# Kernel optimization log

Measured on AMD Instinct MI355X. Metric: run time of the kernel, lower is better.

## Reference

```python
import jax, jax.numpy as jnp
import numpy as np

N = 50000      # nodes
E = 800000     # edges
F = 128        # num_features
H = 128        # hidden_channels
L = 3          # num_layers
P = 32         # num_partitions
EPS = 1e-5     # BatchNorm1d eps


def _batchnorm(h):
    # BatchNorm1d(affine=False, track_running_stats=False): batch stats, biased var
    m = jnp.mean(h, axis=0)
    v = jnp.var(h, axis=0)
    return (h - m) * jax.lax.rsqrt(v + EPS)


def setup_inputs() -> dict:
    key = jax.random.key(0)
    ks = jax.random.split(key, 12)
    x = jax.random.normal(ks[0], (N, F), dtype=jnp.float32)
    edge_index = jax.random.randint(ks[1], (2, E), 0, N)
    edge_weights = jax.random.uniform(ks[2], (E,), dtype=jnp.float32)
    partitions = (jax.random.uniform(ks[3], (N, P)) < (1.0 / P)).astype(jnp.float32)
    node_weights = jax.random.uniform(ks[4], (N,), dtype=jnp.float32)
    edge_curr_node = jax.random.uniform(ks[5], (N,), dtype=jnp.float32)
    conv_w = 0.05 * jax.random.normal(ks[6], (L, F, H), dtype=jnp.float32)
    conv_b = jnp.zeros((L, H), dtype=jnp.float32)
    lin1_w = 0.05 * jax.random.normal(ks[7], (4 * H, H), dtype=jnp.float32)
    lin1_b = jnp.zeros((H,), dtype=jnp.float32)
    lin2_w = 0.05 * jax.random.normal(ks[8], (H, 1), dtype=jnp.float32)
    lin2_b = jnp.zeros((1,), dtype=jnp.float32)
    return {"x": x, "edge_index": edge_index, "edge_weights": edge_weights,
            "partitions": partitions, "node_weights": node_weights,
            "edge_curr_node": edge_curr_node, "conv_w": conv_w, "conv_b": conv_b,
            "lin1_w": lin1_w, "lin1_b": lin1_b, "lin2_w": lin2_w,
            "lin2_b": lin2_b, "curr_node_id": 123}


def reference(x, edge_index, edge_weights, partitions, node_weights,
              edge_curr_node, conv_w, conv_b, lin1_w, lin1_b, lin2_w, lin2_b,
              curr_node_id):
    src, dst = edge_index[0], edge_index[1]
    # GCN normalization with added self-loops (weight 1)
    deg = jax.ops.segment_sum(edge_weights, dst, num_segments=N) + 1.0
    dinv = jax.lax.rsqrt(deg)
    norm = dinv[src] * edge_weights * dinv[dst]          # [E]
    self_norm = (dinv * dinv)[:, None]                   # [N,1]

    h = x
    for l in range(L):
        hw = h @ conv_w[l] + conv_b[l]                   # [N,H]
        agg = jax.ops.segment_sum(hw[src] * norm[:, None], dst, num_segments=N)
        agg = agg + hw * self_norm                       # self-loop term
        h = jax.nn.relu(_batchnorm(agg))

    x_curr = h[curr_node_id]                             # [H]
    # mlp scoring: concat [h | x_curr | edge_col repeated to 2H] -> [N,4H]
    cat = jnp.concatenate([
        h,
        jnp.broadcast_to(x_curr[None, :], (N, H)),
        jnp.broadcast_to(edge_curr_node[:, None], (N, 2 * H)),
    ], axis=1)
    scores = jax.nn.relu(cat @ lin1_w + lin1_b) @ lin2_w + lin2_b  # [N,1]
    # pool == 'sum'
    partition_scores = scores.T @ partitions             # [1,P]
    return (partition_scores, h)
```

## Files before the change

### kernel.cpp

```cpp
#include <hip/hip_runtime.h>

#define N_NODES 50000
#define N_EDGES 800000
#define NP 50048
#define MAXDEG 64
#define PADK 136
#define NCOPY 64
#define EB 3125
#define WPB 512

typedef __bf16 bf16_8 __attribute__((ext_vector_type(8)));
typedef float  f32_4  __attribute__((ext_vector_type(4)));

__device__ inline float2 bf2f2(unsigned int u) {
    union { unsigned int i; float f; } a, b;
    a.i = u << 16;
    b.i = u & 0xffff0000u;
    return make_float2(a.f, b.f);
}

__global__ void k_init_wprep(int* __restrict__ fillp, float* __restrict__ colpart,
                             float* __restrict__ out_head,
                             const float* __restrict__ conv_w, const float* __restrict__ lin1_w,
                             __bf16* __restrict__ WT, float* __restrict__ svec) {
    int b = blockIdx.x;
    if (b < EB) {
        int i = b * 256 + threadIdx.x;
        fillp[i] = 0;
        if (i < 2 * NCOPY * 128) colpart[i] = 0.f;
        if (i < 32) out_head[i] = 0.f;
    } else if (b < EB + WPB) {
        int b2 = b - EB;
        int mat = b2 >> 7, n = b2 & 127, k = threadIdx.x;
        if (k < 128) {
            const float* srcm = (mat < 3) ? (conv_w + (size_t)mat * 16384) : lin1_w;
            WT[((size_t)mat * 128 + n) * 128 + k] = (__bf16)srcm[(size_t)k * 128 + n];
        }
    } else {
        int j = threadIdx.x;
        if (j < 128) {
            float s = 0.f;
            for (int k = 256; k < 512; ++k) s += lin1_w[(size_t)k * 128 + j];
            svec[j] = s;
        }
    }
}

__global__ void k_fillover(const int* __restrict__ src, const int* __restrict__ dst,
                           const float* __restrict__ ew,
                           int* __restrict__ fillp, uint2* __restrict__ esn) {
    int e = blockIdx.x * 256 + threadIdx.x;
    if (e >= N_EDGES) return;
    int d = dst[e];
    int pos = atomicAdd(&fillp[d * 16], 1);
    if (pos < MAXDEG)
        esn[(size_t)d * MAXDEG + pos] = make_uint2((unsigned)src[e], __float_as_uint(ew[e]));
}

__global__ void k_node(const uint2* __restrict__ esn, const int* __restrict__ fillp,
                       float* __restrict__ dinv) {
    int n = blockIdx.x * 256 + threadIdx.x;
    if (n >= N_NODES) return;
    int c = min(fillp[n * 16], MAXDEG);
    float s = 1.0f;
    for (int i = 0; i < c; ++i) s += __uint_as_float(esn[(size_t)n * MAXDEG + i].y);
    dinv[n] = rsqrtf(s);
}

template <int AMODE>
__global__ __launch_bounds__(256) void k_gemm_mfma(const float* __restrict__ A,
                                                   const float* __restrict__ mean,
                                                   const float* __restrict__ rstd,
                                                   const __bf16* __restrict__ WT,
                                                   const float* __restrict__ bias,
                                                   __bf16* __restrict__ C, int nrows) {
    __shared__ __bf16 As[64 * PADK];
    __shared__ __bf16 Ws[128 * PADK];
    int t = threadIdx.x;
    int rowBase = blockIdx.x * 64;
    const uint4* WTg = (const uint4*)WT;
    for (int i = t; i < 2048; i += 256) {
        int n = i >> 4, k8 = i & 15;
        *(uint4*)&Ws[n * PADK + k8 * 8] = WTg[i];
    }
    const float4* A4 = (const float4*)A;
    const float4* M4 = (const float4*)mean;
    const float4* R4 = (const float4*)rstd;
    for (int i = t; i < 1024; i += 256) {
        int r = i >> 4, k8 = i & 15;
        int gr = rowBase + r;
        float4 a0 = make_float4(0.f, 0.f, 0.f, 0.f), a1 = a0;
        if (gr < nrows) {
            a0 = A4[(size_t)gr * 32 + k8 * 2];
            a1 = A4[(size_t)gr * 32 + k8 * 2 + 1];
        }
        if (AMODE == 1) {
            float4 m0 = M4[k8 * 2], m1 = M4[k8 * 2 + 1];
            float4 r0 = R4[k8 * 2], r1 = R4[k8 * 2 + 1];
            a0.x = fmaxf((a0.x - m0.x) * r0.x, 0.f); a0.y = fmaxf((a0.y - m0.y) * r0.y, 0.f);
            a0.z = fmaxf((a0.z - m0.z) * r0.z, 0.f); a0.w = fmaxf((a0.w - m0.w) * r0.w, 0.f);
            a1.x = fmaxf((a1.x - m1.x) * r1.x, 0.f); a1.y = fmaxf((a1.y - m1.y) * r1.y, 0.f);
            a1.z = fmaxf((a1.z - m1.z) * r1.z, 0.f); a1.w = fmaxf((a1.w - m1.w) * r1.w, 0.f);
        }
        bf16_8 o = { (__bf16)a0.x, (__bf16)a0.y, (__bf16)a0.z, (__bf16)a0.w,
                     (__bf16)a1.x, (__bf16)a1.y, (__bf16)a1.z, (__bf16)a1.w };
        *(bf16_8*)&As[r * PADK + k8 * 8] = o;
    }
    __syncthreads();
    int wave = t >> 6, lane = t & 63, quad = lane >> 4, m = lane & 15;
    int ar = wave * 16 + m;
    f32_4 acc[8];
#pragma unroll
    for (int i = 0; i < 8; ++i) acc[i] = (f32_4){0.f, 0.f, 0.f, 0.f};
#pragma unroll
    for (int kk = 0; kk < 4; ++kk) {
        bf16_8 a = *(const bf16_8*)&As[ar * PADK + kk * 32 + quad * 8];
#pragma unroll
        for (int n0 = 0; n0 < 8; ++n0) {
            bf16_8 b = *(const bf16_8*)&Ws[(n0 * 16 + m) * PADK + kk * 32 + quad * 8];
            acc[n0] = __builtin_amdgcn_mfma_f32_16x16x32_bf16(a, b, acc[n0], 0, 0, 0);
        }
    }
    __syncthreads();
#pragma unroll
    for (int n0 = 0; n0 < 8; ++n0) {
        int col = n0 * 16 + m;
        float bi = bias[col];
#pragma unroll
        for (int r = 0; r < 4; ++r) {
            int rr = wave * 16 + quad * 4 + r;
            As[rr * PADK + col] = (__bf16)(acc[n0][r] + bi);
        }
    }
    __syncthreads();
    uint4* Cg = (uint4*)C;
    for (int i = t; i < 1024; i += 256) {
        int r = i >> 4, k8 = i & 15;
        int gr = rowBase + r;
        if (gr < nrows) Cg[(size_t)gr * 16 + k8] = *(const uint4*)&As[r * PADK + k8 * 8];
    }
}

__global__ __launch_bounds__(256) void k_agg(const __bf16* __restrict__ hwb,
                                             const uint2* __restrict__ esn,
                                             const int* __restrict__ fillp,
                                             const float* __restrict__ dinv,
                                             float* __restrict__ agg,
                                             float* __restrict__ colpart) {
    __shared__ float red1[4 * 128], red2[4 * 128];
    int t = threadIdx.x;
    int n = (blockIdx.x * 256 + t) >> 6;
    int lane = t & 63, wave = t >> 6;
    float2 acc = make_float2(0.f, 0.f);
    const unsigned int* hw32 = (const unsigned int*)hwb;
    if (n < N_NODES) {
        float dvn = dinv[n];
        float2 sv = bf2f2(hw32[(size_t)n * 64 + lane]);
        acc.x = sv.x * dvn * dvn; acc.y = sv.y * dvn * dvn;
        int num = min(fillp[n * 16], MAXDEG);
        int s_l = 0; float w_l = 0.f;
        if (lane < num) {
            uint2 e = esn[(size_t)n * MAXDEG + lane];
            s_l = (int)e.x;
            w_l = dinv[s_l] * __uint_as_float(e.y) * dvn;
        }
        int i = 0;
        for (; i + 8 <= num; i += 8) {
            int ss[8]; float ww[8]; unsigned uu[8];
#pragma unroll
            for (int j = 0; j < 8; ++j) { ss[j] = __shfl(s_l, i + j); ww[j] = __shfl(w_l, i + j); }
#pragma unroll
            for (int j = 0; j < 8; ++j) uu[j] = hw32[(size_t)ss[j] * 64 + lane];
#pragma unroll
            for (int j = 0; j < 8; ++j) {
                float2 f = bf2f2(uu[j]);
                acc.x += f.x * ww[j]; acc.y += f.y * ww[j];
            }
        }
        for (; i < num; ++i) {
            int s = __shfl(s_l, i);
            float w = __shfl(w_l, i);
            float2 f = bf2f2(hw32[(size_t)s * 64 + lane]);
            acc.x += f.x * w; acc.y += f.y * w;
        }
        ((float2*)agg)[(size_t)n * 64 + lane] = acc;
    }
    *(float2*)&red1[wave * 128 + 2 * lane] = acc;
    *(float2*)&red2[wave * 128 + 2 * lane] = make_float2(acc.x * acc.x, acc.y * acc.y);
    __syncthreads();
    if (t < 128) {
        float s = red1[t] + red1[128 + t] + red1[256 + t] + red1[384 + t];
        float q = red2[t] + red2[128 + t] + red2[256 + t] + red2[384 + t];
        int c = blockIdx.x & (NCOPY - 1);
        unsafeAtomicAdd(&colpart[c * 128 + t], s);
        unsafeAtomicAdd(&colpart[NCOPY * 128 + c * 128 + t], q);
    }
}

__global__ void k_bnfinal(float* colpart, float* mean, float* rstd) {
    int j = threadIdx.x;
    float s = 0.f, q = 0.f;
    for (int c = 0; c < NCOPY; ++c) {
        s += colpart[c * 128 + j];
        q += colpart[NCOPY * 128 + c * 128 + j];
        colpart[c * 128 + j] = 0.f;
        colpart[NCOPY * 128 + c * 128 + j] = 0.f;
    }
    float m = s * (1.0f / N_NODES);
    float v = q * (1.0f / N_NODES) - m * m;
    mean[j] = m;
    rstd[j] = rsqrtf(v + 1e-5f);
}

__global__ void k_prep(const float* __restrict__ agg, const float* __restrict__ mean,
                       const float* __restrict__ rstd, const int* __restrict__ cid,
                       const float* __restrict__ lin1w, const float* __restrict__ lin1b,
                       float* c0) {
    __shared__ float xc[128];
    int t = threadIdx.x;
    int cn = cid[0];
    float a = agg[(size_t)cn * 128 + t];
    xc[t] = fmaxf((a - mean[t]) * rstd[t], 0.f);
    __syncthreads();
    float acc = lin1b[t];
    for (int k = 0; k < 128; ++k)
        acc += xc[k] * lin1w[(size_t)(128 + k) * 128 + t];
    c0[t] = acc;
}

__global__ __launch_bounds__(256) void k_score_mfma(const float* __restrict__ agg,
                                                    const float* __restrict__ mean,
                                                    const float* __restrict__ rstd,
                                                    const __bf16* __restrict__ WT,
                                                    const float* __restrict__ c0,
                                                    const float* __restrict__ svec,
                                                    const float* __restrict__ ecn,
                                                    const float* __restrict__ lin2w,
                                                    const float* __restrict__ lin2b,
                                                    float* __restrict__ scores,
                                                    float* __restrict__ hout,
                                                    int nrows) {
    __shared__ __bf16 As[64 * PADK];
    __shared__ __bf16 Ws[128 * PADK];
    __shared__ float c0s[128], svs[128], l2s[128];
    int t = threadIdx.x;
    int rowBase = blockIdx.x * 64;
    const uint4* WTg = (const uint4*)WT;
    for (int i = t; i < 2048; i += 256) {
        int n = i >> 4, k8 = i & 15;
        *(uint4*)&Ws[n * PADK + k8 * 8] = WTg[i];
    }
    const float4* A4 = (const float4*)agg;
    const float4* M4 = (const float4*)mean;
    const float4* R4 = (const float4*)rstd;
    float4* H4 = (float4*)hout;
    for (int i = t; i < 1024; i += 256) {
        int r = i >> 4, k8 = i & 15;
        int gr = rowBase + r;
        float4 a0 = make_float4(0.f, 0.f, 0.f, 0.f), a1 = a0;
        if (gr < nrows) {
            a0 = A4[(size_t)gr * 32 + k8 * 2];
            a1 = A4[(size_t)gr * 32 + k8 * 2 + 1];
        }
        float4 m0 = M4[k8 * 2], m1 = M4[k8 * 2 + 1];
        float4 r0 = R4[k8 * 2], r1 = R4[k8 * 2 + 1];
        float4 f0, f1;
        f0.x = fmaxf((a0.x - m0.x) * r0.x, 0.f); f0.y = fmaxf((a0.y - m0.y) * r0.y, 0.f);
        f0.z = fmaxf((a0.z - m0.z) * r0.z, 0.f); f0.w = fmaxf((a0.w - m0.w) * r0.w, 0.f);
        f1.x = fmaxf((a1.x - m1.x) * r1.x, 0.f); f1.y = fmaxf((a1.y - m1.y) * r1.y, 0.f);
        f1.z = fmaxf((a1.z - m1.z) * r1.z, 0.f); f1.w = fmaxf((a1.w - m1.w) * r1.w, 0.f);
        if (gr < nrows) {
            H4[(size_t)gr * 32 + k8 * 2] = f0;
            H4[(size_t)gr * 32 + k8 * 2 + 1] = f1;
        }
        bf16_8 o = { (__bf16)f0.x, (__bf16)f0.y, (__bf16)f0.z, (__bf16)f0.w,
                     (__bf16)f1.x, (__bf16)f1.y, (__bf16)f1.z, (__bf16)f1.w };
        *(bf16_8*)&As[r * PADK + k8 * 8] = o;
    }
    if (t < 128) { c0s[t] = c0[t]; svs[t] = svec[t]; l2s[t] = lin2w[t]; }
    __syncthreads();
    int wave = t >> 6, lane = t & 63, quad = lane >> 4, m = lane & 15;
    int ar = wave * 16 + m;
    f32_4 acc[8];
#pragma unroll
    for (int i = 0; i < 8; ++i) acc[i] = (f32_4){0.f, 0.f, 0.f, 0.f};
#pragma unroll
    for (int kk = 0; kk < 4; ++kk) {
        bf16_8 a = *(const bf16_8*)&As[ar * PADK + kk * 32 + quad * 8];
#pragma unroll
        for (int n0 = 0; n0 < 8; ++n0) {
            bf16_8 b = *(const bf16_8*)&Ws[(n0 * 16 + m) * PADK + kk * 32 + quad * 8];
            acc[n0] = __builtin_amdgcn_mfma_f32_16x16x32_bf16(a, b, acc[n0], 0, 0, 0);
        }
    }
    float l2b = lin2b[0];
#pragma unroll
    for (int r = 0; r < 4; ++r) {
        int row = rowBase + wave * 16 + quad * 4 + r;
        float e = (row < nrows) ? ecn[row] : 0.f;
        float partial = 0.f;
#pragma unroll
        for (int n0 = 0; n0 < 8; ++n0) {
            int col = n0 * 16 + m;
            float v = acc[n0][r] + c0s[col] + e * svs[col];
            partial += fmaxf(v, 0.f) * l2s[col];
        }
        partial += __shfl_xor(partial, 8, 16);
        partial += __shfl_xor(partial, 4, 16);
        partial += __shfl_xor(partial, 2, 16);
        partial += __shfl_xor(partial, 1, 16);
        if (m == 0 && row < nrows) scores[row] = partial + l2b;
    }
}

__global__ void k_partition(const float* __restrict__ scores, const float* __restrict__ part,
                            float* out) {
    __shared__ float red[256];
    int t = threadIdx.x;
    int p = t & 31, rg = t >> 5;
    float acc = 0.f;
    for (int r = blockIdx.x * 8 + rg; r < N_NODES; r += gridDim.x * 8)
        acc += scores[r] * part[(size_t)r * 32 + p];
    red[t] = acc;
    __syncthreads();
    if (t < 32) {
        float s = 0.f;
        for (int i = 0; i < 8; ++i) s += red[i * 32 + t];
        unsafeAtomicAdd(&out[t], s);
    }
}

extern "C" void kernel_launch(void* const* d_in, const int* in_sizes, int n_in,
                              void* d_out, int out_size, void* d_ws, size_t ws_size,
                              hipStream_t stream) {
    const float* x        = (const float*)d_in[0];
    const int*   eidx     = (const int*)d_in[1];
    const float* ew       = (const float*)d_in[2];
    const float* parts    = (const float*)d_in[3];
    const float* ecn      = (const float*)d_in[5];
    const float* conv_w   = (const float*)d_in[6];
    const float* conv_b   = (const float*)d_in[7];
    const float* lin1_w   = (const float*)d_in[8];
    const float* lin1_b   = (const float*)d_in[9];
    const float* lin2_w   = (const float*)d_in[10];
    const float* lin2_b   = (const float*)d_in[11];
    const int*   cid      = (const int*)d_in[12];

    const int* src = eidx;
    const int* dst = eidx + N_EDGES;

    char* p = (char*)d_ws;
    auto alloc = [&](size_t bytes) { char* r = p; p += (bytes + 255) & ~size_t(255); return r; };
    int*    fillp   = (int*)alloc((size_t)N_NODES * 16 * 4);
    uint2*  esn     = (uint2*)alloc((size_t)N_NODES * MAXDEG * 8);
    float*  dinv    = (float*)alloc(NP * 4);
    float*  scores  = (float*)alloc(NP * 4);
    float*  colpart = (float*)alloc(2 * NCOPY * 128 * 4);
    float*  mean    = (float*)alloc(128 * 4);
    float*  rstd    = (float*)alloc(128 * 4);
    float*  c0      = (float*)alloc(128 * 4);
    float*  svec    = (float*)alloc(128 * 4);
    __bf16* WT      = (__bf16*)alloc(4 * 128 * 128 * 2);
    __bf16* hwb     = (__bf16*)alloc((size_t)N_NODES * 128 * 2);
    float*  agg     = (float*)alloc((size_t)N_NODES * 128 * 4);

    float* out_head = (float*)d_out;
    float* hbuf     = (float*)d_out + 32;

    const int NB = (NP + 255) / 256;
    const int GB = (N_NODES + 63) / 64;
    const int AB = (N_NODES * 64 + 255) / 256;

    k_init_wprep<<<EB + WPB + 1, 256, 0, stream>>>(fillp, colpart, out_head,
                                                   conv_w, lin1_w, WT, svec);
    k_fillover<<<EB, 256, 0, stream>>>(src, dst, ew, fillp, esn);
    k_node<<<NB, 256, 0, stream>>>(esn, fillp, dinv);

    for (int l = 0; l < 3; ++l) {
        if (l == 0)
            k_gemm_mfma<0><<<GB, 256, 0, stream>>>(x, mean, rstd, WT, conv_b, hwb, N_NODES);
        else
            k_gemm_mfma<1><<<GB, 256, 0, stream>>>(agg, mean, rstd, WT + (size_t)l * 16384,
                                                   conv_b + (size_t)l * 128, hwb, N_NODES);
        k_agg<<<AB, 256, 0, stream>>>(hwb, esn, fillp, dinv, agg, colpart);
        k_bnfinal<<<1, 128, 0, stream>>>(colpart, mean, rstd);
    }

    k_prep<<<1, 128, 0, stream>>>(agg, mean, rstd, cid, lin1_w, lin1_b, c0);
    k_score_mfma<<<GB, 256, 0, stream>>>(agg, mean, rstd, WT + (size_t)3 * 16384, c0, svec,
                                         ecn, lin2_w, lin2_b, scores, hbuf, N_NODES);
    k_partition<<<256, 256, 0, stream>>>(scores, parts, out_head);
}
```

Measured before the change: 363.3 us.

## Build CSR adjacency via two-pass bucketed sort with shared-memory atomics

Replaces the global-atomic per-edge scatter into padded per-node adjacency lists with a two-stage bucketing. First, edges are grouped by destination into 256-node buckets using block-local counting and staging. Then one block per bucket builds the adjacency lists, degree counts and dinv with shared-memory atomics. This removes the large fillp zeroing, the contended global atomics and the separate degree pass. In exchange it packs src/dst into 16-bit fields, which breaks if node ids reach 65536 (here N is 50000), and it silently drops edges beyond a fixed bucket capacity.

```diff
diff --git a/kernel.cpp b/kernel.cpp
--- a/kernel.cpp
+++ b/kernel.cpp
@@ -6,8 +6,10 @@
 #define MAXDEG 64
 #define PADK 136
 #define NCOPY 64
-#define EB 3125
 #define WPB 512
+#define NBUK 196
+#define BCAP 6144
+#define EBB 782
 
 typedef __bf16 bf16_8 __attribute__((ext_vector_type(8)));
 typedef float  f32_4  __attribute__((ext_vector_type(4)));
@@ -19,52 +21,109 @@
     return make_float2(a.f, b.f);
 }
 
-__global__ void k_init_wprep(int* __restrict__ fillp, float* __restrict__ colpart,
-                             float* __restrict__ out_head,
+__global__ void k_init_wprep(float* __restrict__ colpart, float* __restrict__ out_head,
                              const float* __restrict__ conv_w, const float* __restrict__ lin1_w,
-                             __bf16* __restrict__ WT, float* __restrict__ svec) {
-    int b = blockIdx.x;
-    if (b < EB) {
-        int i = b * 256 + threadIdx.x;
-        fillp[i] = 0;
-        if (i < 2 * NCOPY * 128) colpart[i] = 0.f;
-        if (i < 32) out_head[i] = 0.f;
-    } else if (b < EB + WPB) {
-        int b2 = b - EB;
-        int mat = b2 >> 7, n = b2 & 127, k = threadIdx.x;
-        if (k < 128) {
+                             __bf16* __restrict__ WT, float* __restrict__ svec,
+                             int* __restrict__ bcnt) {
+    int b = blockIdx.x, t = threadIdx.x;
+    if (b < WPB) {
+        int mat = b >> 7, n = b & 127;
+        if (t < 128) {
             const float* srcm = (mat < 3) ? (conv_w + (size_t)mat * 16384) : lin1_w;
-            WT[((size_t)mat * 128 + n) * 128 + k] = (__bf16)srcm[(size_t)k * 128 + n];
-        }
+            WT[((size_t)mat * 128 + n) * 128 + t] = (__bf16)srcm[(size_t)t * 128 + n];
+        }
+    } else if (b == WPB) {
+        if (t < 128) {
+            float s = 0.f;
+            for (int k = 256; k < 512; ++k) s += lin1_w[(size_t)k * 128 + t];
+            svec[t] = s;
+        }
+    } else if (b < WPB + 65) {
+        int i = (b - WPB - 1) * 256 + t;
+        colpart[i] = 0.f;
     } else {
-        int j = threadIdx.x;
-        if (j < 128) {
-            float s = 0.f;
-            for (int k = 256; k < 512; ++k) s += lin1_w[(size_t)k * 128 + j];
-            svec[j] = s;
-        }
-    }
-}
-
-__global__ void k_fillover(const int* __restrict__ src, const int* __restrict__ dst,
-                           const float* __restrict__ ew,
-                           int* __restrict__ fillp, uint2* __restrict__ esn) {
-    int e = blockIdx.x * 256 + threadIdx.x;
-    if (e >= N_EDGES) return;
-    int d = dst[e];
-    int pos = atomicAdd(&fillp[d * 16], 1);
-    if (pos < MAXDEG)
-        esn[(size_t)d * MAXDEG + pos] = make_uint2((unsigned)src[e], __float_as_uint(ew[e]));
-}
-
-__global__ void k_node(const uint2* __restrict__ esn, const int* __restrict__ fillp,
-                       float* __restrict__ dinv) {
-    int n = blockIdx.x * 256 + threadIdx.x;
-    if (n >= N_NODES) return;
-    int c = min(fillp[n * 16], MAXDEG);
-    float s = 1.0f;
-    for (int i = 0; i < c; ++i) s += __uint_as_float(esn[(size_t)n * MAXDEG + i].y);
-    dinv[n] = rsqrtf(s);
+        if (t < 32) out_head[t] = 0.f;
+        for (int i = t; i < NBUK * 16; i += 256) bcnt[i] = 0;
+    }
+}
+
+__global__ __launch_bounds__(1024) void k_bucket(const int* __restrict__ src,
+                                                 const int* __restrict__ dst,
+                                                 const float* __restrict__ ew,
+                                                 int* __restrict__ bcnt,
+                                                 uint2* __restrict__ ebuf) {
+    __shared__ uint2 stage[1024];
+    __shared__ int cnt[NBUK], cnt2[NBUK], lstart[NBUK], gb[NBUK];
+    __shared__ int wtot[4];
+    int t = threadIdx.x;
+    int e0 = blockIdx.x * 1024;
+    int tot = min(1024, N_EDGES - e0);
+    if (t < NBUK) { cnt[t] = 0; cnt2[t] = 0; }
+    __syncthreads();
+    uint2 rec = make_uint2(0u, 0u); int b = -1;
+    if (t < tot) {
+        int e = e0 + t;
+        unsigned s = (unsigned)src[e], d = (unsigned)dst[e];
+        rec = make_uint2(s | (d << 16), __float_as_uint(ew[e]));
+        b = (int)(d >> 8);
+        atomicAdd(&cnt[b], 1);
+    }
+    __syncthreads();
+    int c = (t < NBUK) ? cnt[t] : 0;
+    int x = c;
+#pragma unroll
+    for (int d2 = 1; d2 < 64; d2 <<= 1) {
+        int v = __shfl_up(x, d2, 64);
+        if ((t & 63) >= d2) x += v;
+    }
+    if ((t & 63) == 63 && t < 256) wtot[t >> 6] = x;
+    if (t < NBUK && c > 0) gb[t] = atomicAdd(&bcnt[t * 16], c);
+    __syncthreads();
+    if (t < NBUK) {
+        int pre = x - c;
+        for (int w = 0; w < (t >> 6); ++w) pre += wtot[w];
+        lstart[t] = pre;
+    }
+    __syncthreads();
+    if (t < tot) {
+        int r = atomicAdd(&cnt2[b], 1);
+        stage[lstart[b] + r] = rec;
+    }
+    __syncthreads();
+    if (t < tot) {
+        uint2 v = stage[t];
+        int bb = (int)(v.x >> 24);
+        int idx = gb[bb] + (t - lstart[bb]);
+        if (idx < BCAP) ebuf[(size_t)bb * BCAP + idx] = v;
+    }
+}
+
+__global__ __launch_bounds__(256) void k_build(const int* __restrict__ bcnt,
+                                               const uint2* __restrict__ ebuf,
+                                               uint2* __restrict__ esn,
+                                               int* __restrict__ fillp,
+                                               float* __restrict__ dinv) {
+    __shared__ int cnt[256];
+    __shared__ float wsum[256];
+    int t = threadIdx.x, b = blockIdx.x;
+    cnt[t] = 0; wsum[t] = 0.f;
+    __syncthreads();
+    int m = min(bcnt[b * 16], BCAP);
+    for (int i = t; i < m; i += 256) {
+        uint2 rec = ebuf[(size_t)b * BCAP + i];
+        int d = (int)(rec.x >> 16);
+        int local = d & 255;
+        int pos = atomicAdd(&cnt[local], 1);
+        if (pos < MAXDEG)
+            esn[(size_t)d * MAXDEG + pos] = make_uint2(rec.x & 0xffffu, rec.y);
+        atomicAdd(&wsum[local], __uint_as_float(rec.y));
+    }
+    __syncthreads();
+    int gn = b * 256 + t;
+    if (gn < N_NODES) {
+        fillp[gn] = cnt[t];
+        dinv[gn] = rsqrtf(1.0f + wsum[t]);
+    }
 }
 
 template <int AMODE>
@@ -157,7 +216,7 @@
         float dvn = dinv[n];
         float2 sv = bf2f2(hw32[(size_t)n * 64 + lane]);
         acc.x = sv.x * dvn * dvn; acc.y = sv.y * dvn * dvn;
-        int num = min(fillp[n * 16], MAXDEG);
+        int num = min(fillp[n], MAXDEG);
         int s_l = 0; float w_l = 0.f;
         if (lane < num) {
             uint2 e = esn[(size_t)n * MAXDEG + lane];
@@ -351,7 +410,7 @@
 
     char* p = (char*)d_ws;
     auto alloc = [&](size_t bytes) { char* r = p; p += (bytes + 255) & ~size_t(255); return r; };
-    int*    fillp   = (int*)alloc((size_t)N_NODES * 16 * 4);
+    int*    fillp   = (int*)alloc((size_t)NP * 4);
     uint2*  esn     = (uint2*)alloc((size_t)N_NODES * MAXDEG * 8);
     float*  dinv    = (float*)alloc(NP * 4);
     float*  scores  = (float*)alloc(NP * 4);
@@ -363,18 +422,18 @@
     __bf16* WT      = (__bf16*)alloc(4 * 128 * 128 * 2);
     __bf16* hwb     = (__bf16*)alloc((size_t)N_NODES * 128 * 2);
     float*  agg     = (float*)alloc((size_t)N_NODES * 128 * 4);
+    int*    bcnt    = (int*)alloc((size_t)NBUK * 16 * 4);
+    uint2*  ebuf    = (uint2*)alloc((size_t)NBUK * BCAP * 8);
 
     float* out_head = (float*)d_out;
     float* hbuf     = (float*)d_out + 32;
 
-    const int NB = (NP + 255) / 256;
     const int GB = (N_NODES + 63) / 64;
     const int AB = (N_NODES * 64 + 255) / 256;
 
-    k_init_wprep<<<EB + WPB + 1, 256, 0, stream>>>(fillp, colpart, out_head,
-                                                   conv_w, lin1_w, WT, svec);
-    k_fillover<<<EB, 256, 0, stream>>>(src, dst, ew, fillp, esn);
-    k_node<<<NB, 256, 0, stream>>>(esn, fillp, dinv);
+    k_init_wprep<<<WPB + 66, 256, 0, stream>>>(colpart, out_head, conv_w, lin1_w, WT, svec, bcnt);
+    k_bucket<<<EBB, 1024, 0, stream>>>(src, dst, ew, bcnt, ebuf);
+    k_build<<<NBUK, 256, 0, stream>>>(bcnt, ebuf, esn, fillp, dinv);
 
     for (int l = 0; l < 3; ++l) {
         if (l == 0)
```

New measurement: 341.4 us (median of 2 runs). 6.0% less time.
